# Performance work log

Measured on AMD Instinct MI355X. Metric: run time of the kernel, lower is better.

Reference implementation:

```python
import jax, jax.numpy as jnp
import numpy as np

N_SAMPLES = 131072
N_EVENTS = 128
N_ATOMS = 32
ATOM_SIZE = 512
LATENT = 16
TIME_DIM = 17   # log2(N_SAMPLES)
LAYERS = 7      # log2(N_EVENTS)


def setup_inputs() -> dict:
    key = jax.random.key(0)
    ks = jax.random.split(key, 9)
    u = lambda k, shape, lo, hi: jax.random.uniform(k, shape, jnp.float32, lo, hi)
    return {
        "base_latent": u(ks[0], (1, LATENT), -1.0, 1.0),
        "to_time_W": u(ks[1], (LAYERS, 2 * TIME_DIM * 2, LATENT), -0.02, 0.02),
        "split_W": u(ks[2], (LAYERS, LATENT * 2, LATENT), -0.02, 0.02),
        "split_b": u(ks[3], (LAYERS, LATENT * 2), -0.02, 0.02),
        "atoms": u(ks[4], (N_ATOMS, ATOM_SIZE), -0.01, 0.01),
        "to_atoms_W": u(ks[5], (N_ATOMS, LATENT), -0.02, 0.02),
        "to_atoms_b": u(ks[6], (N_ATOMS,), -0.02, 0.02),
        "to_amp_W": u(ks[7], (1, LATENT), -0.02, 0.02),
        "to_amp_b": u(ks[8], (1,), -0.02, 0.02),
    }


def _sparse_softmax(logits):
    # hard one-hot forward, softmax gradient (straight-through)
    s = jax.nn.softmax(logits, axis=-1)
    hard = jax.nn.one_hot(jnp.argmax(logits, axis=-1), logits.shape[-1], dtype=logits.dtype)
    return hard + s - jax.lax.stop_gradient(s)


def hierarchical_dirac(times):
    # times: (B, E, TIME_DIM, 2) -> (B, E, 2**TIME_DIM) impulse per event
    b, e = times.shape[0], times.shape[1]
    sig = _sparse_softmax(times[:, :, 0, :])           # (B, E, 2)
    for i in range(1, TIME_DIM):
        sel = _sparse_softmax(times[:, :, i, :])       # (B, E, 2)
        sig = (sig[..., :, None] * sel[..., None, :]).reshape(b, e, -1)
    return sig


def fft_convolve(a, b):
    # causal linear convolution of equal-length signals via zero-padded FFT
    n = a.shape[-1]
    fa = jnp.fft.rfft(a, n=2 * n, axis=-1)
    fb = jnp.fft.rfft(b, n=2 * n, axis=-1)
    return jnp.fft.irfft(fa * fb, n=2 * n, axis=-1)[..., :n]


def reference(base_latent, to_time_W, split_W, split_b, atoms,
              to_atoms_W, to_atoms_b, to_amp_W, to_amp_b):
    x = base_latent[:, None, :]                              # (1, 1, L)
    base_times = jnp.zeros((1, 1, TIME_DIM, 2), jnp.float32)
    for i in range(LAYERS):
        b, e, ld = x.shape
        to = (x @ to_time_W[i].T).reshape(b, e, 2, TIME_DIM, 2)
        offsets = base_times[:, :, None, :, :] + to          # scale = 1
        base_times = offsets.reshape(b, e * 2, TIME_DIM, 2)
        x = (x @ split_W[i].T + split_b[i]).reshape(b, e * 2, ld)
    # x: (1, N_EVENTS, L); base_times: (1, N_EVENTS, TIME_DIM, 2)

    # atom synthesis
    a = x @ to_atoms_W.T + to_atoms_b                        # (1, E, N_ATOMS)
    a = a @ atoms                                            # (1, E, ATOM_SIZE)
    n_ = jnp.arange(ATOM_SIZE, dtype=jnp.float32)
    window = 0.54 - 0.46 * jnp.cos(2.0 * jnp.pi * n_ / ATOM_SIZE)  # torch periodic hamming
    a = a * window
    a = jnp.pad(a, ((0, 0), (0, 0), (0, N_SAMPLES - ATOM_SIZE)))
    norm = jnp.linalg.norm(a, axis=-1, keepdims=True)
    a = a / (norm + 1e-8)                                    # unit_norm
    amps = x @ to_amp_W.T + to_amp_b                         # (1, E, 1)
    a = a * amps

    scheduled = hierarchical_dirac(base_times)               # (1, E, N_SAMPLES)
    out = fft_convolve(a, scheduled)                         # (1, E, N_SAMPLES)
    return jnp.sum(out, axis=1, keepdims=True)               # (1, 1, N_SAMPLES)
```

## Files before the change

kernel.cpp:

```cpp
#include <hip/hip_runtime.h>
#include <hip/hip_bf16.h>

#define N_SAMPLES 131072
#define N_EVENTS 128
#define N_ATOMS 32
#define ATOM_SIZE 512
#define LATENT 16
#define TIME_DIM 17
#define LAYERS 7

__device__ __forceinline__ float dot16f(const float* __restrict__ wr,
                                        const float* __restrict__ x) {
    const float4* q = (const float4*)wr;
    float4 a = q[0], b = q[1], c = q[2], d = q[3];
    float s = 0.f;
    s += a.x * x[0]  + a.y * x[1]  + a.z * x[2]  + a.w * x[3];
    s += b.x * x[4]  + b.y * x[5]  + b.z * x[6]  + b.w * x[7];
    s += c.x * x[8]  + c.y * x[9]  + c.z * x[10] + c.w * x[11];
    s += d.x * x[12] + d.y * x[13] + d.z * x[14] + d.w * x[15];
    return s;
}

__global__ __launch_bounds__(64) void expand_kernel(
    const float* __restrict__ base_latent,
    const float* __restrict__ to_time_W,
    const float* __restrict__ split_W,
    const float* __restrict__ split_b,
    const float* __restrict__ atoms,
    const float* __restrict__ to_atoms_W,
    const float* __restrict__ to_atoms_b,
    const float* __restrict__ to_amp_W,
    const float* __restrict__ to_amp_b,
    float* __restrict__ wsA,
    int* __restrict__ wsP)
{
    const int e = blockIdx.x;
    const int t = threadIdx.x;

    __shared__ float x_cur[LATENT];
    __shared__ float x_next[LATENT];
    __shared__ float times[2 * TIME_DIM];
    __shared__ float a32[N_ATOMS];
    __shared__ float s_amp;

    if (t < LATENT) x_cur[t] = base_latent[t];
    if (t < 2 * TIME_DIM) times[t] = 0.f;
    __syncthreads();

    for (int i = 0; i < LAYERS; ++i) {
        const int c = (e >> (6 - i)) & 1;
        if (t < LATENT) {
            const int row = c * LATENT + t;
            x_next[t] = split_b[i * 32 + row] +
                        dot16f(split_W + (i * 32 + row) * LATENT, x_cur);
        } else if (t < LATENT + 2 * TIME_DIM) {
            const int m = t - LATENT;
            const int row = c * (2 * TIME_DIM) + m;
            times[m] += dot16f(to_time_W + (i * 68 + row) * LATENT, x_cur);
        }
        __syncthreads();
        if (t < LATENT) x_cur[t] = x_next[t];
        __syncthreads();
    }

    if (t == 0) {
        int p = 0;
#pragma unroll
        for (int d = 0; d < TIME_DIM; ++d) {
            if (times[2 * d + 1] > times[2 * d]) p |= 1 << (16 - d);
        }
        wsP[e] = p;
        s_amp = to_amp_b[0] + dot16f(to_amp_W, x_cur);
    }
    if (t < N_ATOMS) {
        a32[t] = to_atoms_b[t] + dot16f(to_atoms_W + t * LATENT, x_cur);
    }
    __syncthreads();

    float v[ATOM_SIZE / 64];
    float sumsq = 0.f;
#pragma unroll
    for (int it = 0; it < ATOM_SIZE / 64; ++it) {
        const int col = it * 64 + t;
        float acc = 0.f;
#pragma unroll
        for (int m = 0; m < N_ATOMS; ++m) {
            acc += a32[m] * atoms[m * ATOM_SIZE + col];
        }
        const float wnd =
            0.54f - 0.46f * cosf((float)col * (float)(M_PI / 256.0));
        const float val = wnd * acc;
        sumsq += val * val;
        v[it] = val;
    }
#pragma unroll
    for (int off = 32; off > 0; off >>= 1) sumsq += __shfl_xor(sumsq, off, 64);

    const float scale = s_amp / (sqrtf(sumsq) + 1e-8f);
#pragma unroll
    for (int it = 0; it < ATOM_SIZE / 64; ++it) {
        wsA[e * ATOM_SIZE + it * 64 + t] = v[it] * scale;
    }
}

__global__ __launch_bounds__(256) void gather_kernel(
    const float* __restrict__ wsA,
    const int* __restrict__ wsP,
    float* __restrict__ out)
{
    __shared__ int ev_p[N_EVENTS];
    __shared__ short ev_e[N_EVENTS];
    __shared__ int cnt;

    const int t = threadIdx.x;
    const int k0 = blockIdx.x * 256;

    if (t == 0) cnt = 0;
    __syncthreads();

    if (t < N_EVENTS) {
        const int p = wsP[t];
        if (p + ATOM_SIZE > k0 && p < k0 + 256) {
            const int idx = atomicAdd(&cnt, 1);
            ev_p[idx] = p;
            ev_e[idx] = (short)t;
        }
    }
    __syncthreads();

    const int k = k0 + t;
    float sum = 0.f;
    const int n = cnt;
    for (int i = 0; i < n; ++i) {
        const unsigned d = (unsigned)(k - ev_p[i]);
        if (d < (unsigned)ATOM_SIZE) {
            sum += wsA[(int)ev_e[i] * ATOM_SIZE + (int)d];
        }
    }
    out[k] = sum;
}

extern "C" void kernel_launch(void* const* d_in, const int* in_sizes, int n_in,
                              void* d_out, int out_size, void* d_ws, size_t ws_size,
                              hipStream_t stream)
{
    const float* base_latent = (const float*)d_in[0];
    const float* to_time_W   = (const float*)d_in[1];
    const float* split_W     = (const float*)d_in[2];
    const float* split_b     = (const float*)d_in[3];
    const float* atoms       = (const float*)d_in[4];
    const float* to_atoms_W  = (const float*)d_in[5];
    const float* to_atoms_b  = (const float*)d_in[6];
    const float* to_amp_W    = (const float*)d_in[7];
    const float* to_amp_b    = (const float*)d_in[8];

    float* wsA = (float*)d_ws;
    int*   wsP = (int*)((char*)d_ws + N_EVENTS * ATOM_SIZE * sizeof(float));

    expand_kernel<<<N_EVENTS, 64, 0, stream>>>(
        base_latent, to_time_W, split_W, split_b, atoms,
        to_atoms_W, to_atoms_b, to_amp_W, to_amp_b, wsA, wsP);

    gather_kernel<<<N_SAMPLES / 256, 256, 0, stream>>>(
        wsA, wsP, (float*)d_out);
}
```

Measured before the change: 99.92 us.

## Fuse expand and gather kernels with a grid-wide atomic barrier

```diff
diff --git a/kernel.cpp b/kernel.cpp
--- a/kernel.cpp
+++ b/kernel.cpp
@@ -1,5 +1,4 @@
 #include <hip/hip_runtime.h>
-#include <hip/hip_bf16.h>
 
 #define N_SAMPLES 131072
 #define N_EVENTS 128
@@ -8,6 +7,7 @@
 #define LATENT 16
 #define TIME_DIM 17
 #define LAYERS 7
+#define OUT_PER_BLOCK 1024
 
 __device__ __forceinline__ float dot16f(const float* __restrict__ wr,
                                         const float* __restrict__ x) {
@@ -21,7 +21,7 @@
     return s;
 }
 
-__global__ __launch_bounds__(64) void expand_kernel(
+__global__ __launch_bounds__(256) void fused_kernel(
     const float* __restrict__ base_latent,
     const float* __restrict__ to_time_W,
     const float* __restrict__ split_W,
@@ -32,23 +32,29 @@
     const float* __restrict__ to_amp_W,
     const float* __restrict__ to_amp_b,
     float* __restrict__ wsA,
-    int* __restrict__ wsP)
+    int* __restrict__ wsP,
+    int* __restrict__ wsC,
+    float* __restrict__ out)
 {
-    const int e = blockIdx.x;
+    const int b = blockIdx.x;
     const int t = threadIdx.x;
 
     __shared__ float x_cur[LATENT];
     __shared__ float x_next[LATENT];
     __shared__ float times[2 * TIME_DIM];
     __shared__ float a32[N_ATOMS];
-    __shared__ float s_amp;
+    __shared__ float s_amp, s_scale;
+    __shared__ float wred[4];
+    __shared__ int ev_p[N_EVENTS];
+    __shared__ short ev_e[N_EVENTS];
+    __shared__ int cnt;
 
     if (t < LATENT) x_cur[t] = base_latent[t];
     if (t < 2 * TIME_DIM) times[t] = 0.f;
     __syncthreads();
 
     for (int i = 0; i < LAYERS; ++i) {
-        const int c = (e >> (6 - i)) & 1;
+        const int c = (b >> (6 - i)) & 1;
         if (t < LATENT) {
             const int row = c * LATENT + t;
             x_next[t] = split_b[i * 32 + row] +
@@ -69,7 +75,7 @@
         for (int d = 0; d < TIME_DIM; ++d) {
             if (times[2 * d + 1] > times[2 * d]) p |= 1 << (16 - d);
         }
-        wsP[e] = p;
+        wsP[b] = p;
         s_amp = to_amp_b[0] + dot16f(to_amp_W, x_cur);
     }
     if (t < N_ATOMS) {
@@ -77,50 +83,54 @@
     }
     __syncthreads();
 
-    float v[ATOM_SIZE / 64];
-    float sumsq = 0.f;
-#pragma unroll
-    for (int it = 0; it < ATOM_SIZE / 64; ++it) {
-        const int col = it * 64 + t;
+    float v0, v1, ss = 0.f;
+    {
         float acc = 0.f;
 #pragma unroll
-        for (int m = 0; m < N_ATOMS; ++m) {
-            acc += a32[m] * atoms[m * ATOM_SIZE + col];
-        }
-        const float wnd =
-            0.54f - 0.46f * cosf((float)col * (float)(M_PI / 256.0));
-        const float val = wnd * acc;
-        sumsq += val * val;
-        v[it] = val;
+        for (int m = 0; m < N_ATOMS; ++m) acc += a32[m] * atoms[m * ATOM_SIZE + t];
+        float wnd = 0.54f - 0.46f * cosf((float)t * (float)(M_PI / 256.0));
+        v0 = wnd * acc;
+        ss += v0 * v0;
+
+        acc = 0.f;
+#pragma unroll
+        for (int m = 0; m < N_ATOMS; ++m)
+            acc += a32[m] * atoms[m * ATOM_SIZE + 256 + t];
+        wnd = 0.54f - 0.46f * cosf((float)(t + 256) * (float)(M_PI / 256.0));
+        v1 = wnd * acc;
+        ss += v1 * v1;
     }
 #pragma unroll
-    for (int off = 32; off > 0; off >>= 1) sumsq += __shfl_xor(sumsq, off, 64);
+    for (int off = 32; off > 0; off >>= 1) ss += __shfl_xor(ss, off, 64);
+    if ((t & 63) == 0) wred[t >> 6] = ss;
+    __syncthreads();
+    if (t == 0) {
+        const float tot = wred[0] + wred[1] + wred[2] + wred[3];
+        s_scale = s_amp / (sqrtf(tot) + 1e-8f);
+    }
+    __syncthreads();
+    wsA[b * ATOM_SIZE + t]       = v0 * s_scale;
+    wsA[b * ATOM_SIZE + 256 + t] = v1 * s_scale;
 
-    const float scale = s_amp / (sqrtf(sumsq) + 1e-8f);
-#pragma unroll
-    for (int it = 0; it < ATOM_SIZE / 64; ++it) {
-        wsA[e * ATOM_SIZE + it * 64 + t] = v[it] * scale;
+    __threadfence();
+    __syncthreads();
+    if (t == 0) {
+        __hip_atomic_fetch_add(wsC, 1, __ATOMIC_ACQ_REL, __HIP_MEMORY_SCOPE_AGENT);
+        while (__hip_atomic_load(wsC, __ATOMIC_ACQUIRE, __HIP_MEMORY_SCOPE_AGENT)
+               < (int)gridDim.x) {
+            __builtin_amdgcn_s_sleep(8);
+        }
     }
-}
-
-__global__ __launch_bounds__(256) void gather_kernel(
-    const float* __restrict__ wsA,
-    const int* __restrict__ wsP,
-    float* __restrict__ out)
-{
-    __shared__ int ev_p[N_EVENTS];
-    __shared__ short ev_e[N_EVENTS];
-    __shared__ int cnt;
-
-    const int t = threadIdx.x;
-    const int k0 = blockIdx.x * 256;
+    __syncthreads();
+    __threadfence();
 
     if (t == 0) cnt = 0;
     __syncthreads();
 
+    const int k0 = b * OUT_PER_BLOCK;
     if (t < N_EVENTS) {
         const int p = wsP[t];
-        if (p + ATOM_SIZE > k0 && p < k0 + 256) {
+        if (p + ATOM_SIZE > k0 && p < k0 + OUT_PER_BLOCK) {
             const int idx = atomicAdd(&cnt, 1);
             ev_p[idx] = p;
             ev_e[idx] = (short)t;
@@ -128,16 +138,19 @@
     }
     __syncthreads();
 
-    const int k = k0 + t;
-    float sum = 0.f;
+    const int k = k0 + t * 4;
+    float4 sum = make_float4(0.f, 0.f, 0.f, 0.f);
     const int n = cnt;
     for (int i = 0; i < n; ++i) {
-        const unsigned d = (unsigned)(k - ev_p[i]);
-        if (d < (unsigned)ATOM_SIZE) {
-            sum += wsA[(int)ev_e[i] * ATOM_SIZE + (int)d];
+        const float* __restrict__ src = wsA + (int)ev_e[i] * ATOM_SIZE;
+        const int p = ev_p[i];
+#pragma unroll
+        for (int j = 0; j < 4; ++j) {
+            const unsigned d = (unsigned)(k + j - p);
+            if (d < (unsigned)ATOM_SIZE) (&sum.x)[j] += src[d];
         }
     }
-    out[k] = sum;
+    *(float4*)(out + k) = sum;
 }
 
 extern "C" void kernel_launch(void* const* d_in, const int* in_sizes, int n_in,
@@ -156,11 +169,12 @@
 
     float* wsA = (float*)d_ws;
     int*   wsP = (int*)((char*)d_ws + N_EVENTS * ATOM_SIZE * sizeof(float));
+    int*   wsC = (int*)((char*)d_ws + N_EVENTS * ATOM_SIZE * sizeof(float) + 1024);
 
-    expand_kernel<<<N_EVENTS, 64, 0, stream>>>(
+    hipMemsetAsync(wsC, 0, sizeof(int), stream);
+
+    fused_kernel<<<N_EVENTS, 256, 0, stream>>>(
         base_latent, to_time_W, split_W, split_b, atoms,
-        to_atoms_W, to_atoms_b, to_amp_W, to_amp_b, wsA, wsP);
-
-    gather_kernel<<<N_SAMPLES / 256, 256, 0, stream>>>(
-        wsA, wsP, (float*)d_out);
+        to_atoms_W, to_atoms_b, to_amp_W, to_amp_b,
+        wsA, wsP, wsC, (float*)d_out);
 }
```

Measured after the change: 134.8 us. +34.9%, slower.

## Fuse latent expansion and atom synthesis into the gather kernel, recomputing per block

Applied to the files above, without the earlier changes.

```diff
diff --git a/kernel.cpp b/kernel.cpp
--- a/kernel.cpp
+++ b/kernel.cpp
@@ -1,5 +1,4 @@
 #include <hip/hip_runtime.h>
-#include <hip/hip_bf16.h>
 
 #define N_SAMPLES 131072
 #define N_EVENTS 128
@@ -8,6 +7,7 @@
 #define LATENT 16
 #define TIME_DIM 17
 #define LAYERS 7
+#define TDIM2 (2 * TIME_DIM)
 
 __device__ __forceinline__ float dot16f(const float* __restrict__ wr,
                                         const float* __restrict__ x) {
@@ -21,7 +21,7 @@
     return s;
 }
 
-__global__ __launch_bounds__(64) void expand_kernel(
+__global__ __launch_bounds__(256) void fused_gather_kernel(
     const float* __restrict__ base_latent,
     const float* __restrict__ to_time_W,
     const float* __restrict__ split_W,
@@ -31,110 +31,117 @@
     const float* __restrict__ to_atoms_b,
     const float* __restrict__ to_amp_W,
     const float* __restrict__ to_amp_b,
-    float* __restrict__ wsA,
-    int* __restrict__ wsP)
+    float* __restrict__ out)
 {
-    const int e = blockIdx.x;
     const int t = threadIdx.x;
+    const int k0 = blockIdx.x * 256;
 
-    __shared__ float x_cur[LATENT];
-    __shared__ float x_next[LATENT];
-    __shared__ float times[2 * TIME_DIM];
-    __shared__ float a32[N_ATOMS];
-    __shared__ float s_amp;
+    __shared__ float sx[2][N_EVENTS * LATENT];
+    __shared__ float st[2][N_EVENTS * TDIM2];
+    __shared__ int   sp[N_EVENTS];
+    __shared__ float samp[N_EVENTS];
+    __shared__ int   ev_e[N_EVENTS];
+    __shared__ int   ev_p[N_EVENTS];
+    __shared__ float ev_s[N_EVENTS];
+    __shared__ float wred[4];
+    __shared__ int   cnt;
+    float* a32 = st[0];
 
-    if (t < LATENT) x_cur[t] = base_latent[t];
-    if (t < 2 * TIME_DIM) times[t] = 0.f;
+    if (t < LATENT) sx[0][t] = base_latent[t];
+    else if (t < LATENT + TDIM2) st[0][t - LATENT] = 0.f;
+    if (t == 0) cnt = 0;
     __syncthreads();
 
     for (int i = 0; i < LAYERS; ++i) {
-        const int c = (e >> (6 - i)) & 1;
-        if (t < LATENT) {
-            const int row = c * LATENT + t;
-            x_next[t] = split_b[i * 32 + row] +
-                        dot16f(split_W + (i * 32 + row) * LATENT, x_cur);
-        } else if (t < LATENT + 2 * TIME_DIM) {
-            const int m = t - LATENT;
-            const int row = c * (2 * TIME_DIM) + m;
-            times[m] += dot16f(to_time_W + (i * 68 + row) * LATENT, x_cur);
+        const float* xprev = sx[i & 1];
+        float*       xnext = sx[(i + 1) & 1];
+        const float* tprev = st[i & 1];
+        float*       tnext = st[(i + 1) & 1];
+        const int C = 2 << i;
+        const int rows = C * (LATENT + TDIM2);
+        for (int r = t; r < rows; r += 256) {
+            const int n  = r / 50;
+            const int q  = r - n * 50;
+            const int par = n >> 1, cb = n & 1;
+            const float* xp = xprev + par * LATENT;
+            if (q < LATENT) {
+                xnext[n * LATENT + q] =
+                    split_b[i * 32 + cb * LATENT + q] +
+                    dot16f(split_W + (i * 32 + cb * LATENT + q) * LATENT, xp);
+            } else {
+                const int m = q - LATENT;
+                tnext[n * TDIM2 + m] =
+                    tprev[par * TDIM2 + m] +
+                    dot16f(to_time_W + (i * 68 + cb * TDIM2 + m) * LATENT, xp);
+            }
         }
-        __syncthreads();
-        if (t < LATENT) x_cur[t] = x_next[t];
         __syncthreads();
     }
 
-    if (t == 0) {
+    if (t < N_EVENTS) {
+        const float* te = st[1] + t * TDIM2;
         int p = 0;
 #pragma unroll
         for (int d = 0; d < TIME_DIM; ++d) {
-            if (times[2 * d + 1] > times[2 * d]) p |= 1 << (16 - d);
+            if (te[2 * d + 1] > te[2 * d]) p |= 1 << (16 - d);
         }
-        wsP[e] = p;
-        s_amp = to_amp_b[0] + dot16f(to_amp_W, x_cur);
+        sp[t] = p;
+        samp[t] = to_amp_b[0] + dot16f(to_amp_W, sx[1] + t * LATENT);
     }
-    if (t < N_ATOMS) {
-        a32[t] = to_atoms_b[t] + dot16f(to_atoms_W + t * LATENT, x_cur);
+    for (int r = t; r < N_EVENTS * N_ATOMS; r += 256) {
+        const int e = r >> 5, m = r & 31;
+        a32[e * N_ATOMS + m] =
+            to_atoms_b[m] + dot16f(to_atoms_W + m * LATENT, sx[1] + e * LATENT);
     }
     __syncthreads();
 
-    float v[ATOM_SIZE / 64];
-    float sumsq = 0.f;
-#pragma unroll
-    for (int it = 0; it < ATOM_SIZE / 64; ++it) {
-        const int col = it * 64 + t;
-        float acc = 0.f;
-#pragma unroll
-        for (int m = 0; m < N_ATOMS; ++m) {
-            acc += a32[m] * atoms[m * ATOM_SIZE + col];
-        }
-        const float wnd =
-            0.54f - 0.46f * cosf((float)col * (float)(M_PI / 256.0));
-        const float val = wnd * acc;
-        sumsq += val * val;
-        v[it] = val;
-    }
-#pragma unroll
-    for (int off = 32; off > 0; off >>= 1) sumsq += __shfl_xor(sumsq, off, 64);
-
-    const float scale = s_amp / (sqrtf(sumsq) + 1e-8f);
-#pragma unroll
-    for (int it = 0; it < ATOM_SIZE / 64; ++it) {
-        wsA[e * ATOM_SIZE + it * 64 + t] = v[it] * scale;
-    }
-}
-
-__global__ __launch_bounds__(256) void gather_kernel(
-    const float* __restrict__ wsA,
-    const int* __restrict__ wsP,
-    float* __restrict__ out)
-{
-    __shared__ int ev_p[N_EVENTS];
-    __shared__ short ev_e[N_EVENTS];
-    __shared__ int cnt;
-
-    const int t = threadIdx.x;
-    const int k0 = blockIdx.x * 256;
-
-    if (t == 0) cnt = 0;
-    __syncthreads();
-
     if (t < N_EVENTS) {
-        const int p = wsP[t];
+        const int p = sp[t];
         if (p + ATOM_SIZE > k0 && p < k0 + 256) {
             const int idx = atomicAdd(&cnt, 1);
+            ev_e[idx] = t;
             ev_p[idx] = p;
-            ev_e[idx] = (short)t;
         }
     }
     __syncthreads();
+    const int n = cnt;
+
+    for (int i = 0; i < n; ++i) {
+        const float* ae = a32 + ev_e[i] * N_ATOMS;
+        float acc0 = 0.f, acc1 = 0.f;
+#pragma unroll
+        for (int m = 0; m < N_ATOMS; ++m) {
+            acc0 += ae[m] * atoms[m * ATOM_SIZE + t];
+            acc1 += ae[m] * atoms[m * ATOM_SIZE + 256 + t];
+        }
+        const float w0 = 0.54f - 0.46f * cosf((float)t * (float)(M_PI / 256.0));
+        const float w1 =
+            0.54f - 0.46f * cosf((float)(t + 256) * (float)(M_PI / 256.0));
+        const float v0 = w0 * acc0, v1 = w1 * acc1;
+        float ss = v0 * v0 + v1 * v1;
+#pragma unroll
+        for (int off = 32; off > 0; off >>= 1) ss += __shfl_xor(ss, off, 64);
+        if ((t & 63) == 0) wred[t >> 6] = ss;
+        __syncthreads();
+        if (t == 0) {
+            const float tot = wred[0] + wred[1] + wred[2] + wred[3];
+            ev_s[i] = samp[ev_e[i]] / (sqrtf(tot) + 1e-8f);
+        }
+        __syncthreads();
+    }
 
     const int k = k0 + t;
     float sum = 0.f;
-    const int n = cnt;
     for (int i = 0; i < n; ++i) {
         const unsigned d = (unsigned)(k - ev_p[i]);
         if (d < (unsigned)ATOM_SIZE) {
-            sum += wsA[(int)ev_e[i] * ATOM_SIZE + (int)d];
+            const float* ae = a32 + ev_e[i] * N_ATOMS;
+            float acc = 0.f;
+#pragma unroll
+            for (int m = 0; m < N_ATOMS; ++m) acc += ae[m] * atoms[m * ATOM_SIZE + d];
+            const float wnd =
+                0.54f - 0.46f * cosf((float)d * (float)(M_PI / 256.0));
+            sum += wnd * acc * ev_s[i];
         }
     }
     out[k] = sum;
@@ -154,13 +161,7 @@
     const float* to_amp_W    = (const float*)d_in[7];
     const float* to_amp_b    = (const float*)d_in[8];
 
-    float* wsA = (float*)d_ws;
-    int*   wsP = (int*)((char*)d_ws + N_EVENTS * ATOM_SIZE * sizeof(float));
-
-    expand_kernel<<<N_EVENTS, 64, 0, stream>>>(
+    fused_gather_kernel<<<N_SAMPLES / 256, 256, 0, stream>>>(
         base_latent, to_time_W, split_W, split_b, atoms,
-        to_atoms_W, to_atoms_b, to_amp_W, to_amp_b, wsA, wsP);
-
-    gather_kernel<<<N_SAMPLES / 256, 256, 0, stream>>>(
-        wsA, wsP, (float*)d_out);
+        to_atoms_W, to_atoms_b, to_amp_W, to_amp_b, (float*)d_out);
 }
```

Result: slower. 181.6 us (+81.8%).
